# Kernel optimization log

Measured on AMD Instinct MI355X. Metric: run time of the kernel, lower is better.

## Reference

```python
import jax, jax.numpy as jnp
import numpy as np

BLOCK_SIZE_KV = 16
SCALE = 0.08838834764831845  # 1/sqrt(128)


def setup_inputs() -> dict:
    key = jax.random.key(0)
    k0, k1, k2, k3, k4 = jax.random.split(key, 5)
    B, H, D, KVH = 32, 32, 128, 8
    MAX_BLOCKS = 256                 # 4096-token max context / 16-token pages
    N_PHYS_BLOCKS = B * MAX_BLOCKS   # 8192 physical pages
    q = jax.random.normal(k0, (B, H, D), jnp.float32)
    k_cache = jax.random.normal(k1, (N_PHYS_BLOCKS, BLOCK_SIZE_KV, KVH, D), jnp.float32)
    v_cache = jax.random.normal(k2, (N_PHYS_BLOCKS, BLOCK_SIZE_KV, KVH, D), jnp.float32)
    # each logical page maps to a distinct physical page (vLLM-style allocation)
    block_tables = jax.random.permutation(k3, N_PHYS_BLOCKS).reshape(B, MAX_BLOCKS).astype(jnp.int32)
    context_lens = jax.random.randint(k4, (B,), 1, MAX_BLOCKS * BLOCK_SIZE_KV + 1, jnp.int32)
    return {"q": q, "k_cache": k_cache, "v_cache": v_cache,
            "block_tables": block_tables, "context_lens": context_lens}


def reference(q, k_cache, v_cache, block_tables, context_lens):
    # q: [B, H, D]; k/v_cache: [NB, 16, KVH, D]; block_tables: [B, MB]; context_lens: [B]
    B, H, D = q.shape
    KVH = k_cache.shape[2]
    G = H // KVH                                  # GQA group size
    MB = block_tables.shape[1]
    S = MB * BLOCK_SIZE_KV                        # max logical context
    # gather paged KV per sequence: [B, MB, 16, KVH, D] -> [B, S, KVH, D]
    K = k_cache[block_tables].reshape(B, S, KVH, D)
    V = v_cache[block_tables].reshape(B, S, KVH, D)
    qg = q.reshape(B, KVH, G, D)
    scores = jnp.einsum('bkgd,bskd->bkgs', qg, K) * jnp.float32(SCALE)
    valid = (jnp.arange(S)[None, :] < context_lens[:, None])  # [B, S]
    scores = jnp.where(valid[:, None, None, :], scores, -jnp.inf)
    p = jax.nn.softmax(scores, axis=-1)           # online-softmax equivalent
    out = jnp.einsum('bkgs,bskd->bkgd', p, V).reshape(B, H, D)
    return out
```

## Files before the change

### kernel.cpp

```cpp
#include <hip/hip_runtime.h>


constexpr int Dh   = 128;
constexpr int Gq   = 4;
constexpr int KVH  = 8;
constexpr int Hq   = 32;
constexpr int Bb   = 32;
constexpr int MB   = 256;
constexpr int PAGE = 16;
constexpr float SCALE = 0.08838834764831845f;

constexpr int NPARTS = 16;
constexpr int PART_TOKENS = 256;

constexpr int PART_STRIDE = Gq * Dh + 2 * Gq;

__global__ __launch_bounds__(256, 4)
void attn_partial(const float* __restrict__ q,
                  const float* __restrict__ kc,
                  const float* __restrict__ vc,
                  const int*   __restrict__ bt,
                  const int*   __restrict__ cl,
                  float*       __restrict__ ws)
{
    const int blk  = blockIdx.x;
    const int part = blk % NPARTS;
    const int bkv  = blk / NPARTS;
    const int kvh  = bkv % KVH;
    const int b    = bkv / KVH;

    const int ctx    = cl[b];
    const int pstart = part * PART_TOKENS;
    if (pstart >= ctx) return;
    const int n = min(PART_TOKENS, ctx - pstart);

    const int tid  = threadIdx.x;
    const int wave = tid >> 6;
    const int lane = tid & 63;
    const int tl   = lane >> 4;
    const int dc   = lane & 15;

    __shared__ float v_s[64][Dh];
    __shared__ float sc_s[64][5];
    __shared__ float alpha_s[Gq];

    float4 qa[Gq], qb[Gq];
    {
        const float* qbase = q + ((size_t)(b * Hq + kvh * Gq)) * Dh + dc * 8;
        #pragma unroll
        for (int g = 0; g < Gq; ++g) {
            qa[g] = *(const float4*)(qbase + g * Dh);
            qb[g] = *(const float4*)(qbase + g * Dh + 4);
        }
    }

    const int d0 = lane * 2;
    float accx = 0.f, accy = 0.f;

    float m_run = -1e30f, l_run = 0.f;

    const int* btrow = bt + b * MB;
    const int page0  = pstart >> 4;
    const int iters  = (n + 63) >> 6;

    for (int it = 0; it < iters; ++it) {
        const int page_local = it * 4 + wave;
        const int tok_base   = page_local * PAGE;
        const int phys       = btrow[page0 + page_local];
        const float* kp = kc + (((size_t)phys * PAGE) * KVH + kvh) * Dh;
        const float* vp = vc + (((size_t)phys * PAGE) * KVH + kvh) * Dh;

        #pragma unroll
        for (int si = 0; si < 4; ++si) {
            const int tk = si * 4 + tl;
            const float* kt = kp + (size_t)tk * (KVH * Dh) + dc * 8;
            const float* vt = vp + (size_t)tk * (KVH * Dh) + dc * 8;
            float4 ka = *(const float4*)kt;
            float4 kb = *(const float4*)(kt + 4);
            float4 va = *(const float4*)vt;
            float4 vb = *(const float4*)(vt + 4);

            const int slot = wave * PAGE + tk;
            *(float4*)&v_s[slot][dc * 8]     = va;
            *(float4*)&v_s[slot][dc * 8 + 4] = vb;

            const bool valid = (tok_base + tk) < n;
            #pragma unroll
            for (int g = 0; g < Gq; ++g) {
                float s = ka.x * qa[g].x + ka.y * qa[g].y + ka.z * qa[g].z + ka.w * qa[g].w
                        + kb.x * qb[g].x + kb.y * qb[g].y + kb.z * qb[g].z + kb.w * qb[g].w;
                s += __shfl_xor(s, 1);
                s += __shfl_xor(s, 2);
                s += __shfl_xor(s, 4);
                s += __shfl_xor(s, 8);
                if (dc == 0)
                    sc_s[slot][g] = valid ? s * SCALE : -1e30f;
            }
        }
        __syncthreads();

        {
            float s = sc_s[lane][wave];
            float tm = s;
            tm = fmaxf(tm, __shfl_xor(tm, 1));
            tm = fmaxf(tm, __shfl_xor(tm, 2));
            tm = fmaxf(tm, __shfl_xor(tm, 4));
            tm = fmaxf(tm, __shfl_xor(tm, 8));
            tm = fmaxf(tm, __shfl_xor(tm, 16));
            tm = fmaxf(tm, __shfl_xor(tm, 32));
            const float m_new = fmaxf(m_run, tm);
            const float p = __expf(s - m_new);
            float ls = p;
            ls += __shfl_xor(ls, 1);
            ls += __shfl_xor(ls, 2);
            ls += __shfl_xor(ls, 4);
            ls += __shfl_xor(ls, 8);
            ls += __shfl_xor(ls, 16);
            ls += __shfl_xor(ls, 32);
            const float alpha = __expf(m_run - m_new);
            l_run = l_run * alpha + ls;
            m_run = m_new;
            sc_s[lane][wave] = p;
            if (lane == 0) alpha_s[wave] = alpha;
        }
        __syncthreads();

        {
            const float a = alpha_s[wave];
            accx *= a; accy *= a;
            #pragma unroll 8
            for (int t = 0; t < 64; ++t) {
                const float p = sc_s[t][wave];
                const float2 v = *(const float2*)&v_s[t][d0];
                accx = fmaf(p, v.x, accx);
                accy = fmaf(p, v.y, accy);
            }
        }
        __syncthreads();
    }

    float* wp = ws + ((size_t)bkv * NPARTS + part) * PART_STRIDE;
    wp[wave * Dh + d0]     = accx;
    wp[wave * Dh + d0 + 1] = accy;
    if (lane == 0) {
        wp[Gq * Dh + wave]      = m_run;
        wp[Gq * Dh + Gq + wave] = l_run;
    }
}

__global__ __launch_bounds__(256, 4)
void attn_reduce(const float* __restrict__ ws,
                 const int*   __restrict__ cl,
                 float*       __restrict__ out)
{
    const int bkv = blockIdx.x;
    const int kvh = bkv % KVH;
    const int b   = bkv / KVH;
    const int ctx = cl[b];
    const int np  = min(NPARTS, (ctx + PART_TOKENS - 1) / PART_TOKENS);

    const int tid = threadIdx.x;
    const int g   = tid >> 6;
    const int d0  = (tid & 63) * 2;

    const float* base = ws + (size_t)bkv * NPARTS * PART_STRIDE;

    float m = -1e30f;
    for (int p = 0; p < np; ++p)
        m = fmaxf(m, base[p * PART_STRIDE + Gq * Dh + g]);

    float L = 0.f, ax = 0.f, ay = 0.f;
    for (int p = 0; p < np; ++p) {
        const float* bp = base + p * PART_STRIDE;
        const float c = __expf(bp[Gq * Dh + g] - m);
        L  += bp[Gq * Dh + Gq + g] * c;
        ax += bp[g * Dh + d0]     * c;
        ay += bp[g * Dh + d0 + 1] * c;
    }
    const float inv = 1.f / L;
    const size_t o = ((size_t)(b * Hq + kvh * Gq + g)) * Dh + d0;
    out[o]     = ax * inv;
    out[o + 1] = ay * inv;
}

extern "C" void kernel_launch(void* const* d_in, const int* in_sizes, int n_in,
                              void* d_out, int out_size, void* d_ws, size_t ws_size,
                              hipStream_t stream) {
    const float* q  = (const float*)d_in[0];
    const float* kc = (const float*)d_in[1];
    const float* vc = (const float*)d_in[2];
    const int*   bt = (const int*)d_in[3];
    const int*   cl = (const int*)d_in[4];
    float* out = (float*)d_out;
    float* ws  = (float*)d_ws;

    dim3 blk(256);
    attn_partial<<<dim3(Bb * KVH * NPARTS), blk, 0, stream>>>(q, kc, vc, bt, cl, ws);
    attn_reduce<<<dim3(Bb * KVH), blk, 0, stream>>>(ws, cl, out);
}
```

Before: 176.0 us.

## Make each wave own a partition with register double-buffered page loads

Each wavefront now processes its own 128-token partition independently, with no shared memory and no block-level barriers. The next page's K and V are prefetched into registers while the current page is computed, and softmax state and accumulators for all four query heads are kept per lane and reduced across lanes with shuffles at the end. SCALE is folded into q and the partition count doubles, which gives more parallel work but also more partial results for the reduce kernel. Register pressure rises sharply (launch bounds lowered to 2), and waves that exit early can leave blocks partly idle.

```diff
diff --git a/kernel.cpp b/kernel.cpp
--- a/kernel.cpp
+++ b/kernel.cpp
@@ -10,12 +10,15 @@
 constexpr int PAGE = 16;
 constexpr float SCALE = 0.08838834764831845f;
 
-constexpr int NPARTS = 16;
-constexpr int PART_TOKENS = 256;
+constexpr int NPARTS      = 32;
+constexpr int PART_TOKENS = 128;
+constexpr int PG_STRIDE   = PAGE * KVH * Dh;
 
 constexpr int PART_STRIDE = Gq * Dh + 2 * Gq;
 
-__global__ __launch_bounds__(256, 4)
+struct PageR { float4 a[4], b[4]; };
+
+__global__ __launch_bounds__(256, 2)
 void attn_partial(const float* __restrict__ q,
                   const float* __restrict__ kc,
                   const float* __restrict__ vc,
@@ -23,128 +26,143 @@
                   const int*   __restrict__ cl,
                   float*       __restrict__ ws)
 {
-    const int blk  = blockIdx.x;
-    const int part = blk % NPARTS;
-    const int bkv  = blk / NPARTS;
-    const int kvh  = bkv % KVH;
-    const int b    = bkv / KVH;
+    const int wid  = blockIdx.x * 4 + (threadIdx.x >> 6);
+    const int part = wid & (NPARTS - 1);
+    const int bkv  = wid >> 5;
+    const int kvh  = bkv & (KVH - 1);
+    const int b    = bkv >> 3;
 
     const int ctx    = cl[b];
     const int pstart = part * PART_TOKENS;
     if (pstart >= ctx) return;
-    const int n = min(PART_TOKENS, ctx - pstart);
-
-    const int tid  = threadIdx.x;
-    const int wave = tid >> 6;
-    const int lane = tid & 63;
+    const int n   = min(PART_TOKENS, ctx - pstart);
+    const int npg = (n + PAGE - 1) >> 4;
+
+    const int lane = threadIdx.x & 63;
     const int tl   = lane >> 4;
     const int dc   = lane & 15;
 
-    __shared__ float v_s[64][Dh];
-    __shared__ float sc_s[64][5];
-    __shared__ float alpha_s[Gq];
-
     float4 qa[Gq], qb[Gq];
     {
-        const float* qbase = q + ((size_t)(b * Hq + kvh * Gq)) * Dh + dc * 8;
+        const float* qbase = q + (size_t)(b * Hq + kvh * Gq) * Dh + dc * 8;
         #pragma unroll
         for (int g = 0; g < Gq; ++g) {
-            qa[g] = *(const float4*)(qbase + g * Dh);
-            qb[g] = *(const float4*)(qbase + g * Dh + 4);
-        }
-    }
-
-    const int d0 = lane * 2;
-    float accx = 0.f, accy = 0.f;
-
-    float m_run = -1e30f, l_run = 0.f;
-
-    const int* btrow = bt + b * MB;
-    const int page0  = pstart >> 4;
-    const int iters  = (n + 63) >> 6;
-
-    for (int it = 0; it < iters; ++it) {
-        const int page_local = it * 4 + wave;
-        const int tok_base   = page_local * PAGE;
-        const int phys       = btrow[page0 + page_local];
-        const float* kp = kc + (((size_t)phys * PAGE) * KVH + kvh) * Dh;
-        const float* vp = vc + (((size_t)phys * PAGE) * KVH + kvh) * Dh;
-
+            float4 x = *(const float4*)(qbase + g * Dh);
+            float4 y = *(const float4*)(qbase + g * Dh + 4);
+            qa[g] = make_float4(x.x * SCALE, x.y * SCALE, x.z * SCALE, x.w * SCALE);
+            qb[g] = make_float4(y.x * SCALE, y.y * SCALE, y.z * SCALE, y.w * SCALE);
+        }
+    }
+
+    const int* btrow = bt + b * MB + (pstart >> 4);
+    const int lane_off = tl * (KVH * Dh) + kvh * Dh + dc * 8;
+
+    float4 accA[Gq], accB[Gq];
+    float  m_run[Gq], l_run[Gq];
+    #pragma unroll
+    for (int g = 0; g < Gq; ++g) {
+        accA[g] = make_float4(0.f, 0.f, 0.f, 0.f);
+        accB[g] = make_float4(0.f, 0.f, 0.f, 0.f);
+        m_run[g] = -1e30f;
+        l_run[g] = 0.f;
+    }
+
+    auto LOAD = [&](PageR& K, PageR& V, int p) {
+        const int phys = btrow[p];
+        const float* kp = kc + (size_t)phys * PG_STRIDE + lane_off;
+        const float* vp = vc + (size_t)phys * PG_STRIDE + lane_off;
         #pragma unroll
         for (int si = 0; si < 4; ++si) {
-            const int tk = si * 4 + tl;
-            const float* kt = kp + (size_t)tk * (KVH * Dh) + dc * 8;
-            const float* vt = vp + (size_t)tk * (KVH * Dh) + dc * 8;
-            float4 ka = *(const float4*)kt;
-            float4 kb = *(const float4*)(kt + 4);
-            float4 va = *(const float4*)vt;
-            float4 vb = *(const float4*)(vt + 4);
-
-            const int slot = wave * PAGE + tk;
-            *(float4*)&v_s[slot][dc * 8]     = va;
-            *(float4*)&v_s[slot][dc * 8 + 4] = vb;
-
-            const bool valid = (tok_base + tk) < n;
+            K.a[si] = *(const float4*)(kp + si * 4 * (KVH * Dh));
+            K.b[si] = *(const float4*)(kp + si * 4 * (KVH * Dh) + 4);
+            V.a[si] = *(const float4*)(vp + si * 4 * (KVH * Dh));
+            V.b[si] = *(const float4*)(vp + si * 4 * (KVH * Dh) + 4);
+        }
+    };
+
+    auto COMPUTE = [&](const PageR& K, const PageR& V, int p) {
+        float s[4][Gq];
+        #pragma unroll
+        for (int si = 0; si < 4; ++si) {
+            const bool valid = (p * PAGE + si * 4 + tl) < n;
             #pragma unroll
             for (int g = 0; g < Gq; ++g) {
-                float s = ka.x * qa[g].x + ka.y * qa[g].y + ka.z * qa[g].z + ka.w * qa[g].w
-                        + kb.x * qb[g].x + kb.y * qb[g].y + kb.z * qb[g].z + kb.w * qb[g].w;
-                s += __shfl_xor(s, 1);
-                s += __shfl_xor(s, 2);
-                s += __shfl_xor(s, 4);
-                s += __shfl_xor(s, 8);
-                if (dc == 0)
-                    sc_s[slot][g] = valid ? s * SCALE : -1e30f;
+                float t = K.a[si].x * qa[g].x + K.a[si].y * qa[g].y
+                        + K.a[si].z * qa[g].z + K.a[si].w * qa[g].w
+                        + K.b[si].x * qb[g].x + K.b[si].y * qb[g].y
+                        + K.b[si].z * qb[g].z + K.b[si].w * qb[g].w;
+                t += __shfl_xor(t, 1);
+                t += __shfl_xor(t, 2);
+                t += __shfl_xor(t, 4);
+                t += __shfl_xor(t, 8);
+                s[si][g] = valid ? t : -1e30f;
             }
         }
-        __syncthreads();
-
-        {
-            float s = sc_s[lane][wave];
-            float tm = s;
-            tm = fmaxf(tm, __shfl_xor(tm, 1));
-            tm = fmaxf(tm, __shfl_xor(tm, 2));
-            tm = fmaxf(tm, __shfl_xor(tm, 4));
-            tm = fmaxf(tm, __shfl_xor(tm, 8));
+        #pragma unroll
+        for (int g = 0; g < Gq; ++g) {
+            float tm = fmaxf(fmaxf(s[0][g], s[1][g]), fmaxf(s[2][g], s[3][g]));
             tm = fmaxf(tm, __shfl_xor(tm, 16));
             tm = fmaxf(tm, __shfl_xor(tm, 32));
-            const float m_new = fmaxf(m_run, tm);
-            const float p = __expf(s - m_new);
-            float ls = p;
-            ls += __shfl_xor(ls, 1);
-            ls += __shfl_xor(ls, 2);
-            ls += __shfl_xor(ls, 4);
-            ls += __shfl_xor(ls, 8);
+            const float mn    = fmaxf(m_run[g], tm);
+            const float alpha = __expf(m_run[g] - mn);
+            m_run[g] = mn;
+            const float p0 = __expf(s[0][g] - mn);
+            const float p1 = __expf(s[1][g] - mn);
+            const float p2 = __expf(s[2][g] - mn);
+            const float p3 = __expf(s[3][g] - mn);
+            float ls = p0 + p1 + p2 + p3;
             ls += __shfl_xor(ls, 16);
             ls += __shfl_xor(ls, 32);
-            const float alpha = __expf(m_run - m_new);
-            l_run = l_run * alpha + ls;
-            m_run = m_new;
-            sc_s[lane][wave] = p;
-            if (lane == 0) alpha_s[wave] = alpha;
-        }
-        __syncthreads();
-
-        {
-            const float a = alpha_s[wave];
-            accx *= a; accy *= a;
-            #pragma unroll 8
-            for (int t = 0; t < 64; ++t) {
-                const float p = sc_s[t][wave];
-                const float2 v = *(const float2*)&v_s[t][d0];
-                accx = fmaf(p, v.x, accx);
-                accy = fmaf(p, v.y, accy);
-            }
-        }
-        __syncthreads();
+            l_run[g] = l_run[g] * alpha + ls;
+            accA[g].x = fmaf(p3, V.a[3].x, fmaf(p2, V.a[2].x, fmaf(p1, V.a[1].x, fmaf(p0, V.a[0].x, accA[g].x * alpha))));
+            accA[g].y = fmaf(p3, V.a[3].y, fmaf(p2, V.a[2].y, fmaf(p1, V.a[1].y, fmaf(p0, V.a[0].y, accA[g].y * alpha))));
+            accA[g].z = fmaf(p3, V.a[3].z, fmaf(p2, V.a[2].z, fmaf(p1, V.a[1].z, fmaf(p0, V.a[0].z, accA[g].z * alpha))));
+            accA[g].w = fmaf(p3, V.a[3].w, fmaf(p2, V.a[2].w, fmaf(p1, V.a[1].w, fmaf(p0, V.a[0].w, accA[g].w * alpha))));
+            accB[g].x = fmaf(p3, V.b[3].x, fmaf(p2, V.b[2].x, fmaf(p1, V.b[1].x, fmaf(p0, V.b[0].x, accB[g].x * alpha))));
+            accB[g].y = fmaf(p3, V.b[3].y, fmaf(p2, V.b[2].y, fmaf(p1, V.b[1].y, fmaf(p0, V.b[0].y, accB[g].y * alpha))));
+            accB[g].z = fmaf(p3, V.b[3].z, fmaf(p2, V.b[2].z, fmaf(p1, V.b[1].z, fmaf(p0, V.b[0].z, accB[g].z * alpha))));
+            accB[g].w = fmaf(p3, V.b[3].w, fmaf(p2, V.b[2].w, fmaf(p1, V.b[1].w, fmaf(p0, V.b[0].w, accB[g].w * alpha))));
+        }
+    };
+
+    PageR K0, V0, K1, V1;
+    LOAD(K0, V0, 0);
+    int p = 0;
+    while (true) {
+        if (p + 1 < npg) LOAD(K1, V1, p + 1);
+        COMPUTE(K0, V0, p);
+        ++p; if (p >= npg) break;
+        if (p + 1 < npg) LOAD(K0, V0, p + 1);
+        COMPUTE(K1, V1, p);
+        ++p; if (p >= npg) break;
+    }
+
+    #pragma unroll
+    for (int g = 0; g < Gq; ++g) {
+        accA[g].x += __shfl_xor(accA[g].x, 16); accA[g].x += __shfl_xor(accA[g].x, 32);
+        accA[g].y += __shfl_xor(accA[g].y, 16); accA[g].y += __shfl_xor(accA[g].y, 32);
+        accA[g].z += __shfl_xor(accA[g].z, 16); accA[g].z += __shfl_xor(accA[g].z, 32);
+        accA[g].w += __shfl_xor(accA[g].w, 16); accA[g].w += __shfl_xor(accA[g].w, 32);
+        accB[g].x += __shfl_xor(accB[g].x, 16); accB[g].x += __shfl_xor(accB[g].x, 32);
+        accB[g].y += __shfl_xor(accB[g].y, 16); accB[g].y += __shfl_xor(accB[g].y, 32);
+        accB[g].z += __shfl_xor(accB[g].z, 16); accB[g].z += __shfl_xor(accB[g].z, 32);
+        accB[g].w += __shfl_xor(accB[g].w, 16); accB[g].w += __shfl_xor(accB[g].w, 32);
     }
 
     float* wp = ws + ((size_t)bkv * NPARTS + part) * PART_STRIDE;
-    wp[wave * Dh + d0]     = accx;
-    wp[wave * Dh + d0 + 1] = accy;
+    #pragma unroll
+    for (int g = 0; g < Gq; ++g) {
+        if (tl == g) {
+            *(float4*)(wp + g * Dh + dc * 8)     = accA[g];
+            *(float4*)(wp + g * Dh + dc * 8 + 4) = accB[g];
+        }
+    }
     if (lane == 0) {
-        wp[Gq * Dh + wave]      = m_run;
-        wp[Gq * Dh + Gq + wave] = l_run;
+        #pragma unroll
+        for (int g = 0; g < Gq; ++g) {
+            wp[Gq * Dh + g]      = m_run[g];
+            wp[Gq * Dh + Gq + g] = l_run[g];
+        }
     }
 }
 
@@ -154,8 +172,8 @@
                  float*       __restrict__ out)
 {
     const int bkv = blockIdx.x;
-    const int kvh = bkv % KVH;
-    const int b   = bkv / KVH;
+    const int kvh = bkv & (KVH - 1);
+    const int b   = bkv >> 3;
     const int ctx = cl[b];
     const int np  = min(NPARTS, (ctx + PART_TOKENS - 1) / PART_TOKENS);
 
@@ -194,7 +212,9 @@
     float* out = (float*)d_out;
     float* ws  = (float*)d_ws;
 
-    dim3 blk(256);
-    attn_partial<<<dim3(Bb * KVH * NPARTS), blk, 0, stream>>>(q, kc, vc, bt, cl, ws);
-    attn_reduce<<<dim3(Bb * KVH), blk, 0, stream>>>(ws, cl, out);
+    const int nwaves  = Bb * KVH * NPARTS;
+    const int nblocks = nwaves / 4;
+
+    attn_partial<<<dim3(nblocks), dim3(256), 0, stream>>>(q, kc, vc, bt, cl, ws);
+    attn_reduce<<<dim3(Bb * KVH), dim3(256), 0, stream>>>(ws, cl, out);
 }
```

After: 244.0 us. +38.6%, slower.
